# Kernel optimization log

Measured on AMD Instinct MI355X. Metric: run time of the kernel, lower is better.

Reference implementation:

```python
import jax, jax.numpy as jnp
import numpy as np

T = 10          # time_steps
IN_DIM = 784    # 28*28
HID = 256
NCLS = 47
THRESH = 1.0
TAU_MEM = 2.0   # LIF membrane time constant
TAU_OUT = 2.0   # readout EMA time constant


@jax.custom_vjp
def spike_fn(u):
    # Heaviside spike on (v - threshold), surrogate gradient in bwd.
    return (u >= 0.0).astype(u.dtype)

def _spike_fwd(u):
    return spike_fn(u), u

def _spike_bwd(u, g):
    # sigmoid surrogate derivative, slope 4
    s = jax.nn.sigmoid(4.0 * u)
    return (g * 4.0 * s * (1.0 - s),)

spike_fn.defvjp(_spike_fwd, _spike_bwd)


def setup_inputs() -> dict:
    key = jax.random.key(0)
    k1, k2, k3 = jax.random.split(key, 3)
    x = jax.random.uniform(k1, (4096, 1, 28, 28), dtype=jnp.float32)
    W1 = jax.random.normal(k2, (IN_DIM, HID), dtype=jnp.float32) / np.float32(np.sqrt(IN_DIM))
    b1 = jnp.zeros((HID,), jnp.float32)
    Wr = jax.random.normal(k3, (HID, NCLS), dtype=jnp.float32) / np.float32(np.sqrt(HID))
    br = jnp.zeros((NCLS,), jnp.float32)
    return {"x": x, "W1": W1, "b1": b1, "Wr": Wr, "br": br}


def reference(x, W1, b1, Wr, br):
    B = x.shape[0]
    xf = x.reshape(B, -1)  # [B, 784] pixel intensities in [0,1]
    # rate_encode_flat: Bernoulli(p=pixel) spikes per timestep -> [T, B, 784]
    ek = jax.random.key(42)
    seq = (jax.random.uniform(ek, (T, B, IN_DIM), dtype=xf.dtype) < xf[None]).astype(xf.dtype)

    def step(carry, s_t):
        v_hid, v_out = carry
        I_hid = s_t @ W1 + b1                      # [B, HID]
        v_hid = v_hid + (I_hid - v_hid) / TAU_MEM  # leaky integration
        spk = spike_fn(v_hid - THRESH)             # spike emission
        v_hid = v_hid * (1.0 - spk)                # hard reset to 0
        I = spk @ Wr + br                          # [B, NCLS]
        v_out = v_out + (I - v_out) / TAU_OUT      # output EMA
        return (v_hid, v_out), None

    init = (jnp.zeros((B, HID), xf.dtype), jnp.zeros((B, NCLS), xf.dtype))
    (_, v_out), _ = jax.lax.scan(step, init, seq)
    return v_out
```

## Files before the change

### kernel.cpp

```cpp
#include <hip/hip_runtime.h>
#include <stdint.h>


#define T_STEPS 10
#define BATCH   4096
#define IN_DIM  784
#define HID     256
#define NCLS    47
#define NROWS   (T_STEPS * BATCH)
#define KWORDS  25
#define KPAD    800

#define WS_IALL_OFF 0u
#define WS_G_OFF    46039040u
#define WS_W1HI_OFF WS_G_OFF
#define WS_W1MD_OFF (WS_G_OFF + 409600u)
#define WS_W1LO_OFF (WS_G_OFF + 819200u)

typedef __attribute__((ext_vector_type(8))) short    bf16x8;
typedef __attribute__((ext_vector_type(4))) float    f32x4;
typedef __attribute__((ext_vector_type(4))) uint32_t u32x4;

__device__ __forceinline__ uint32_t rotl32(uint32_t x, uint32_t r) {
    return __builtin_amdgcn_alignbit(x, x, 32u - r);
}

__device__ __forceinline__ uint32_t tf_hash(uint32_t lo) {
    const uint32_t ks0 = 0u;
    const uint32_t ks1 = 42u;
    const uint32_t ks2 = 0x1BD11BDAu ^ 0u ^ 42u;
    uint32_t x0 = 0u + ks0;
    uint32_t x1 = lo + ks1;
#define TF_RND(r) { x0 += x1; x1 = rotl32(x1, r); x1 ^= x0; }
    TF_RND(13) TF_RND(15) TF_RND(26) TF_RND(6)
    x0 += ks1; x1 += ks2 + 1u;
    TF_RND(17) TF_RND(29) TF_RND(16) TF_RND(24)
    x0 += ks2; x1 += ks0 + 2u;
    TF_RND(13) TF_RND(15) TF_RND(26) TF_RND(6)
    x0 += ks0; x1 += ks1 + 3u;
    TF_RND(17) TF_RND(29) TF_RND(16) TF_RND(24)
    x0 += ks1; x1 += ks2 + 4u;
    TF_RND(13) TF_RND(15) TF_RND(26) TF_RND(6)
    x0 += ks2; x1 += ks0 + 5u;
#undef TF_RND
    return x0 ^ x1;
}

__global__ __launch_bounds__(256) void splitk_k(
        const float* __restrict__ W1, ushort* __restrict__ hiT,
        ushort* __restrict__ midT, ushort* __restrict__ loT) {
    int n = blockIdx.x;
    for (int k = threadIdx.x; k < KPAD; k += 256) {
        float w = (k < IN_DIM) ? W1[k * HID + n] : 0.0f;
        uint32_t u = __float_as_uint(w);
        uint32_t hb = (u + 0x7FFFu + ((u >> 16) & 1u)) >> 16;
        float hf = __uint_as_float(hb << 16);
        float r1 = w - hf;
        uint32_t u1 = __float_as_uint(r1);
        uint32_t mb = (u1 + 0x7FFFu + ((u1 >> 16) & 1u)) >> 16;
        float mf2 = __uint_as_float(mb << 16);
        float r2 = r1 - mf2;
        uint32_t u2 = __float_as_uint(r2);
        uint32_t lb = (u2 + 0x7FFFu + ((u2 >> 16) & 1u)) >> 16;
        hiT [n * KPAD + k] = (ushort)hb;
        midT[n * KPAD + k] = (ushort)mb;
        loT [n * KPAD + k] = (ushort)lb;
    }
}

#define LDS_A  0
#define LDS_BH 4096
#define LDS_BM 20480
#define LDS_BL 36864

__global__ __launch_bounds__(256, 3) void fused_gemm_k(
        const ushort* __restrict__ hiT, const ushort* __restrict__ midT,
        const ushort* __restrict__ loT, const float* __restrict__ b1,
        const float* __restrict__ x, float* __restrict__ I_all) {
    __shared__ __align__(16) char lds[53248];

    const int tid = threadIdx.x;
    const int l   = tid & 63;
    const int wv  = tid >> 6;
    const int t   = blockIdx.x >> 6;
    const int b0  = (blockIdx.x & 63) << 6;
    const int m0  = blockIdx.x << 6;

    f32x4 acc[4][4] = {};

    const int q   = l >> 4;
    const int sig = q ^ (l & 3) ^ ((l >> 2) & 3);
    const int a_base = LDS_A + ((l & 15) << 6) + (sig << 4);
    const int b_off  = (((wv << 6) + (l & 15)) << 6) + (sig << 4);

    const int er = tid >> 2;
    const int eq = tid & 3;
    const int ea = LDS_A + (er << 6) + ((eq ^ (er & 3) ^ ((er >> 2) & 3)) << 4);
    const int row_b = b0 + er;
    const float* xrow = x + (size_t)row_b * IN_DIM;
    const uint32_t ibase = (uint32_t)(row_b * IN_DIM)
                         + (uint32_t)t * (uint32_t)(BATCH * IN_DIM);

    for (int kw = 0; kw < KWORDS; ++kw) {
        __syncthreads();

#pragma unroll
        for (int i = 0; i < 4; ++i) {
            int s  = (wv << 8) + (i << 6) + l;
            int n  = s >> 2;
            int qs = s & 3;
            int qd = qs ^ (n & 3) ^ ((n >> 2) & 3);
            size_t gb = (size_t)n * (KPAD * 2) + ((size_t)kw << 6) + ((size_t)qd << 4);
            int ldst = ((wv << 8) + (i << 6)) << 4;
            __builtin_amdgcn_global_load_lds(
                (const __attribute__((address_space(1))) void*)((const char*)hiT + gb),
                (__attribute__((address_space(3))) void*)(lds + LDS_BH + ldst),
                16, 0, 0);
            __builtin_amdgcn_global_load_lds(
                (const __attribute__((address_space(1))) void*)((const char*)midT + gb),
                (__attribute__((address_space(3))) void*)(lds + LDS_BM + ldst),
                16, 0, 0);
            __builtin_amdgcn_global_load_lds(
                (const __attribute__((address_space(1))) void*)((const char*)loT + gb),
                (__attribute__((address_space(3))) void*)(lds + LDS_BL + ldst),
                16, 0, 0);
        }

        {
            u32x4 v = {0u, 0u, 0u, 0u};
            if (!(kw == 24 && eq >= 2)) {
                const int k0 = (kw << 5) + (eq << 3);
                float4 xa = *(const float4*)&xrow[k0];
                float4 xb = *(const float4*)&xrow[k0 + 4];
                const uint32_t ib = ibase + (uint32_t)k0;
                uint32_t c0 = ((float)(tf_hash(ib + 0u) >> 9) < xa.x * 8388608.0f) ? 0x3F80u : 0u;
                uint32_t c1 = ((float)(tf_hash(ib + 1u) >> 9) < xa.y * 8388608.0f) ? 0x3F800000u : 0u;
                uint32_t c2 = ((float)(tf_hash(ib + 2u) >> 9) < xa.z * 8388608.0f) ? 0x3F80u : 0u;
                uint32_t c3 = ((float)(tf_hash(ib + 3u) >> 9) < xa.w * 8388608.0f) ? 0x3F800000u : 0u;
                uint32_t c4 = ((float)(tf_hash(ib + 4u) >> 9) < xb.x * 8388608.0f) ? 0x3F80u : 0u;
                uint32_t c5 = ((float)(tf_hash(ib + 5u) >> 9) < xb.y * 8388608.0f) ? 0x3F800000u : 0u;
                uint32_t c6 = ((float)(tf_hash(ib + 6u) >> 9) < xb.z * 8388608.0f) ? 0x3F80u : 0u;
                uint32_t c7 = ((float)(tf_hash(ib + 7u) >> 9) < xb.w * 8388608.0f) ? 0x3F800000u : 0u;
                v.x = c0 | c1;  v.y = c2 | c3;  v.z = c4 | c5;  v.w = c6 | c7;
            }
            *(u32x4*)(lds + ea) = v;
        }

        __syncthreads();

        bf16x8 af[4];
#pragma unroll
        for (int mt = 0; mt < 4; ++mt)
            af[mt] = *(const bf16x8*)(lds + a_base + (mt << 10));
#pragma unroll
        for (int nt = 0; nt < 4; ++nt) {
            bf16x8 bh = *(const bf16x8*)(lds + LDS_BH + b_off + (nt << 10));
            bf16x8 bm = *(const bf16x8*)(lds + LDS_BM + b_off + (nt << 10));
            bf16x8 bl = *(const bf16x8*)(lds + LDS_BL + b_off + (nt << 10));
#pragma unroll
            for (int mt = 0; mt < 4; ++mt) {
                acc[mt][nt] = __builtin_amdgcn_mfma_f32_16x16x32_bf16(af[mt], bh, acc[mt][nt], 0, 0, 0);
                acc[mt][nt] = __builtin_amdgcn_mfma_f32_16x16x32_bf16(af[mt], bm, acc[mt][nt], 0, 0, 0);
                acc[mt][nt] = __builtin_amdgcn_mfma_f32_16x16x32_bf16(af[mt], bl, acc[mt][nt], 0, 0, 0);
            }
        }
    }

    const int c0 = l & 15;
    float b1v[4];
#pragma unroll
    for (int nt = 0; nt < 4; ++nt)
        b1v[nt] = b1[(wv << 6) + (nt << 4) + c0];
#pragma unroll
    for (int mt = 0; mt < 4; ++mt) {
#pragma unroll
        for (int nt = 0; nt < 4; ++nt) {
            int col = (wv << 6) + (nt << 4) + c0;
#pragma unroll
            for (int r = 0; r < 4; ++r) {
                int row = m0 + (mt << 4) + (q << 2) + r;
                I_all[(size_t)row * HID + col] = acc[mt][nt][r] + b1v[nt];
            }
        }
    }
}

__global__ __launch_bounds__(256) void scan_k(
        const float* __restrict__ I_all, float* __restrict__ g) {
    int b = blockIdx.x;
    int h = threadIdx.x;
    const float* p = I_all + ((size_t)b << 8) + h;
    float v = 0.f, ga = 0.f, wt = 0.0009765625f;
#pragma unroll
    for (int t = 0; t < T_STEPS; ++t) {
        float I = p[(size_t)t * BATCH * HID];
        v = v + (I - v) * 0.5f;
        if (v >= 1.0f) { ga += wt; v = 0.f; }
        wt += wt;
    }
    g[(b << 8) + h] = ga;
}

__global__ __launch_bounds__(256) void out_k(
        const float* __restrict__ g, const float* __restrict__ Wr,
        const float* __restrict__ br, float* __restrict__ out) {
    __shared__ float gl[4 * 256];
    int tid = threadIdx.x;
    int b0 = blockIdx.x << 2;
    *(float4*)&gl[tid << 2] = *(const float4*)&g[(b0 << 8) + (tid << 2)];
    __syncthreads();
    int row = tid >> 6;
    int c = tid & 63;
    if (c >= NCLS) return;
    const float* grow = &gl[row << 8];
    float acc = 0.f;
#pragma unroll 4
    for (int h = 0; h < HID; ++h)
        acc = fmaf(grow[h], Wr[h * NCLS + c], acc);
    out[(b0 + row) * NCLS + c] = acc + br[c] * 0.9990234375f;
}

extern "C" void kernel_launch(void* const* d_in, const int* in_sizes, int n_in,
                              void* d_out, int out_size, void* d_ws, size_t ws_size,
                              hipStream_t stream) {
    const float* x  = (const float*)d_in[0];
    const float* W1 = (const float*)d_in[1];
    const float* b1 = (const float*)d_in[2];
    const float* Wr = (const float*)d_in[3];
    const float* br = (const float*)d_in[4];
    float* out = (float*)d_out;

    float*    I_all = (float*)   ((char*)d_ws + WS_IALL_OFF);
    float*    g     = (float*)   ((char*)d_ws + WS_G_OFF);
    ushort*   w1hi  = (ushort*)  ((char*)d_ws + WS_W1HI_OFF);
    ushort*   w1md  = (ushort*)  ((char*)d_ws + WS_W1MD_OFF);
    ushort*   w1lo  = (ushort*)  ((char*)d_ws + WS_W1LO_OFF);

    splitk_k<<<HID, 256, 0, stream>>>(W1, w1hi, w1md, w1lo);
    fused_gemm_k<<<NROWS / 64, 256, 0, stream>>>(w1hi, w1md, w1lo, b1, x, I_all);
    scan_k<<<BATCH, 256, 0, stream>>>(I_all, g);
    out_k<<<BATCH / 4, 256, 0, stream>>>(g, Wr, br, out);
}
```

Baseline: 209.7 us.

## Double-buffer hashed input slab, inline-asm threefry rotates, fuse scan with readout

The GEMM kernel now double-buffers the Bernoulli-encoded A tile in LDS. The hash for the next k-slab is computed while the current slab's MFMAs run, so each iteration still uses two barriers but with less serialization. The threefry rotations use inline v_alignbit asm with precomputed shift amounts, and the zero key additions are dropped. The LIF scan and the readout matmul are merged into one kernel that handles 16 batch rows per block, which removes the g buffer round trip and one launch. In exchange, LDS use grows and occupancy may drop.

Measured after the change: 231.9 us. 1.11x slower.

```diff
diff --git a/kernel.cpp b/kernel.cpp
--- a/kernel.cpp
+++ b/kernel.cpp
@@ -12,37 +12,34 @@
 #define KPAD    800
 
 #define WS_IALL_OFF 0u
-#define WS_G_OFF    46039040u
-#define WS_W1HI_OFF WS_G_OFF
-#define WS_W1MD_OFF (WS_G_OFF + 409600u)
-#define WS_W1LO_OFF (WS_G_OFF + 819200u)
+#define WS_W1HI_OFF 46039040u
+#define WS_W1MD_OFF (46039040u + 409600u)
+#define WS_W1LO_OFF (46039040u + 819200u)
 
 typedef __attribute__((ext_vector_type(8))) short    bf16x8;
 typedef __attribute__((ext_vector_type(4))) float    f32x4;
 typedef __attribute__((ext_vector_type(4))) uint32_t u32x4;
 
-__device__ __forceinline__ uint32_t rotl32(uint32_t x, uint32_t r) {
-    return __builtin_amdgcn_alignbit(x, x, 32u - r);
-}
+#define TF_RND(s32mr) {                                             \
+    x0 += x1;                                                       \
+    asm("v_alignbit_b32 %0, %1, %1, " s32mr : "=v"(x1) : "v"(x1));  \
+    x1 ^= x0; }
 
 __device__ __forceinline__ uint32_t tf_hash(uint32_t lo) {
-    const uint32_t ks0 = 0u;
     const uint32_t ks1 = 42u;
-    const uint32_t ks2 = 0x1BD11BDAu ^ 0u ^ 42u;
-    uint32_t x0 = 0u + ks0;
+    const uint32_t ks2 = 0x1BD11BDAu ^ 42u;
+    uint32_t x0 = 0u;
     uint32_t x1 = lo + ks1;
-#define TF_RND(r) { x0 += x1; x1 = rotl32(x1, r); x1 ^= x0; }
-    TF_RND(13) TF_RND(15) TF_RND(26) TF_RND(6)
+    TF_RND("19") TF_RND("17") TF_RND("6")  TF_RND("26")
     x0 += ks1; x1 += ks2 + 1u;
-    TF_RND(17) TF_RND(29) TF_RND(16) TF_RND(24)
-    x0 += ks2; x1 += ks0 + 2u;
-    TF_RND(13) TF_RND(15) TF_RND(26) TF_RND(6)
-    x0 += ks0; x1 += ks1 + 3u;
-    TF_RND(17) TF_RND(29) TF_RND(16) TF_RND(24)
+    TF_RND("15") TF_RND("3")  TF_RND("16") TF_RND("8")
+    x0 += ks2; x1 += 2u;
+    TF_RND("19") TF_RND("17") TF_RND("6")  TF_RND("26")
+    x1 += ks1 + 3u;
+    TF_RND("15") TF_RND("3")  TF_RND("16") TF_RND("8")
     x0 += ks1; x1 += ks2 + 4u;
-    TF_RND(13) TF_RND(15) TF_RND(26) TF_RND(6)
-    x0 += ks2; x1 += ks0 + 5u;
-#undef TF_RND
+    TF_RND("19") TF_RND("17") TF_RND("6")  TF_RND("26")
+    x0 += ks2; x1 += 5u;
     return x0 ^ x1;
 }
 
@@ -68,16 +65,17 @@
     }
 }
 
-#define LDS_A  0
-#define LDS_BH 4096
-#define LDS_BM 20480
-#define LDS_BL 36864
+#define LDS_A0 0
+#define LDS_A1 4096
+#define LDS_BH 8192
+#define LDS_BM 24576
+#define LDS_BL 40960
 
 __global__ __launch_bounds__(256, 3) void fused_gemm_k(
         const ushort* __restrict__ hiT, const ushort* __restrict__ midT,
         const ushort* __restrict__ loT, const float* __restrict__ b1,
         const float* __restrict__ x, float* __restrict__ I_all) {
-    __shared__ __align__(16) char lds[53248];
+    __shared__ __align__(16) char lds[57344];
 
     const int tid = threadIdx.x;
     const int l   = tid & 63;
@@ -90,16 +88,38 @@
 
     const int q   = l >> 4;
     const int sig = q ^ (l & 3) ^ ((l >> 2) & 3);
-    const int a_base = LDS_A + ((l & 15) << 6) + (sig << 4);
+    const int a_base = ((l & 15) << 6) + (sig << 4);
     const int b_off  = (((wv << 6) + (l & 15)) << 6) + (sig << 4);
 
     const int er = tid >> 2;
     const int eq = tid & 3;
-    const int ea = LDS_A + (er << 6) + ((eq ^ (er & 3) ^ ((er >> 2) & 3)) << 4);
+    const int ea = (er << 6) + ((eq ^ (er & 3) ^ ((er >> 2) & 3)) << 4);
     const int row_b = b0 + er;
     const float* xrow = x + (size_t)row_b * IN_DIM;
     const uint32_t ibase = (uint32_t)(row_b * IN_DIM)
                          + (uint32_t)t * (uint32_t)(BATCH * IN_DIM);
+
+    auto hash_slab = [&](int kwt, char* dst) {
+        u32x4 v = {0u, 0u, 0u, 0u};
+        if (!(kwt == 24 && eq >= 2)) {
+            const int k0 = (kwt << 5) + (eq << 3);
+            float4 xa = *(const float4*)&xrow[k0];
+            float4 xb = *(const float4*)&xrow[k0 + 4];
+            const uint32_t ib = ibase + (uint32_t)k0;
+            uint32_t c0 = ((float)(tf_hash(ib + 0u) >> 9) < xa.x * 8388608.0f) ? 0x3F80u : 0u;
+            uint32_t c1 = ((float)(tf_hash(ib + 1u) >> 9) < xa.y * 8388608.0f) ? 0x3F800000u : 0u;
+            uint32_t c2 = ((float)(tf_hash(ib + 2u) >> 9) < xa.z * 8388608.0f) ? 0x3F80u : 0u;
+            uint32_t c3 = ((float)(tf_hash(ib + 3u) >> 9) < xa.w * 8388608.0f) ? 0x3F800000u : 0u;
+            uint32_t c4 = ((float)(tf_hash(ib + 4u) >> 9) < xb.x * 8388608.0f) ? 0x3F80u : 0u;
+            uint32_t c5 = ((float)(tf_hash(ib + 5u) >> 9) < xb.y * 8388608.0f) ? 0x3F800000u : 0u;
+            uint32_t c6 = ((float)(tf_hash(ib + 6u) >> 9) < xb.z * 8388608.0f) ? 0x3F80u : 0u;
+            uint32_t c7 = ((float)(tf_hash(ib + 7u) >> 9) < xb.w * 8388608.0f) ? 0x3F800000u : 0u;
+            v.x = c0 | c1;  v.y = c2 | c3;  v.z = c4 | c5;  v.w = c6 | c7;
+        }
+        *(u32x4*)dst = v;
+    };
+
+    hash_slab(0, lds + LDS_A0 + ea);
 
     for (int kw = 0; kw < KWORDS; ++kw) {
         __syncthreads();
@@ -126,32 +146,16 @@
                 16, 0, 0);
         }
 
-        {
-            u32x4 v = {0u, 0u, 0u, 0u};
-            if (!(kw == 24 && eq >= 2)) {
-                const int k0 = (kw << 5) + (eq << 3);
-                float4 xa = *(const float4*)&xrow[k0];
-                float4 xb = *(const float4*)&xrow[k0 + 4];
-                const uint32_t ib = ibase + (uint32_t)k0;
-                uint32_t c0 = ((float)(tf_hash(ib + 0u) >> 9) < xa.x * 8388608.0f) ? 0x3F80u : 0u;
-                uint32_t c1 = ((float)(tf_hash(ib + 1u) >> 9) < xa.y * 8388608.0f) ? 0x3F800000u : 0u;
-                uint32_t c2 = ((float)(tf_hash(ib + 2u) >> 9) < xa.z * 8388608.0f) ? 0x3F80u : 0u;
-                uint32_t c3 = ((float)(tf_hash(ib + 3u) >> 9) < xa.w * 8388608.0f) ? 0x3F800000u : 0u;
-                uint32_t c4 = ((float)(tf_hash(ib + 4u) >> 9) < xb.x * 8388608.0f) ? 0x3F80u : 0u;
-                uint32_t c5 = ((float)(tf_hash(ib + 5u) >> 9) < xb.y * 8388608.0f) ? 0x3F800000u : 0u;
-                uint32_t c6 = ((float)(tf_hash(ib + 6u) >> 9) < xb.z * 8388608.0f) ? 0x3F80u : 0u;
-                uint32_t c7 = ((float)(tf_hash(ib + 7u) >> 9) < xb.w * 8388608.0f) ? 0x3F800000u : 0u;
-                v.x = c0 | c1;  v.y = c2 | c3;  v.z = c4 | c5;  v.w = c6 | c7;
-            }
-            *(u32x4*)(lds + ea) = v;
-        }
+        if (kw + 1 < KWORDS)
+            hash_slab(kw + 1, lds + ((kw & 1) ? LDS_A0 : LDS_A1) + ea);
 
         __syncthreads();
 
+        const char* abuf = lds + ((kw & 1) ? LDS_A1 : LDS_A0);
         bf16x8 af[4];
 #pragma unroll
         for (int mt = 0; mt < 4; ++mt)
-            af[mt] = *(const bf16x8*)(lds + a_base + (mt << 10));
+            af[mt] = *(const bf16x8*)(abuf + a_base + (mt << 10));
 #pragma unroll
         for (int nt = 0; nt < 4; ++nt) {
             bf16x8 bh = *(const bf16x8*)(lds + LDS_BH + b_off + (nt << 10));
@@ -185,39 +189,50 @@
     }
 }
 
-__global__ __launch_bounds__(256) void scan_k(
-        const float* __restrict__ I_all, float* __restrict__ g) {
-    int b = blockIdx.x;
-    int h = threadIdx.x;
-    const float* p = I_all + ((size_t)b << 8) + h;
-    float v = 0.f, ga = 0.f, wt = 0.0009765625f;
-#pragma unroll
-    for (int t = 0; t < T_STEPS; ++t) {
-        float I = p[(size_t)t * BATCH * HID];
-        v = v + (I - v) * 0.5f;
-        if (v >= 1.0f) { ga += wt; v = 0.f; }
-        wt += wt;
-    }
-    g[(b << 8) + h] = ga;
-}
-
-__global__ __launch_bounds__(256) void out_k(
-        const float* __restrict__ g, const float* __restrict__ Wr,
+__global__ __launch_bounds__(256) void scanout_k(
+        const float* __restrict__ I_all, const float* __restrict__ Wr,
         const float* __restrict__ br, float* __restrict__ out) {
-    __shared__ float gl[4 * 256];
-    int tid = threadIdx.x;
-    int b0 = blockIdx.x << 2;
-    *(float4*)&gl[tid << 2] = *(const float4*)&g[(b0 << 8) + (tid << 2)];
+    __shared__ float gl[16 * 256];
+    const int tid = threadIdx.x;
+    const int b0  = blockIdx.x << 4;
+
+#pragma unroll 4
+    for (int b = 0; b < 16; ++b) {
+        const float* p = I_all + ((size_t)(b0 + b) << 8) + tid;
+        float v = 0.f, ga = 0.f, wt = 0.0009765625f;
+#pragma unroll
+        for (int t = 0; t < T_STEPS; ++t) {
+            float I = p[(size_t)t * BATCH * HID];
+            v = v + (I - v) * 0.5f;
+            if (v >= 1.0f) { ga += wt; v = 0.f; }
+            wt += wt;
+        }
+        gl[(b << 8) + tid] = ga;
+    }
     __syncthreads();
-    int row = tid >> 6;
-    int c = tid & 63;
+
+    const int wv = tid >> 6;
+    const int c  = tid & 63;
     if (c >= NCLS) return;
-    const float* grow = &gl[row << 8];
-    float acc = 0.f;
-#pragma unroll 4
-    for (int h = 0; h < HID; ++h)
-        acc = fmaf(grow[h], Wr[h * NCLS + c], acc);
-    out[(b0 + row) * NCLS + c] = acc + br[c] * 0.9990234375f;
+    float acc[4] = {0.f, 0.f, 0.f, 0.f};
+    for (int h4 = 0; h4 < 64; ++h4) {
+        float w0 = Wr[((h4 << 2) + 0) * NCLS + c];
+        float w1 = Wr[((h4 << 2) + 1) * NCLS + c];
+        float w2 = Wr[((h4 << 2) + 2) * NCLS + c];
+        float w3 = Wr[((h4 << 2) + 3) * NCLS + c];
+#pragma unroll
+        for (int j = 0; j < 4; ++j) {
+            float4 gg = *(float4*)&gl[(((wv << 2) + j) << 8) + (h4 << 2)];
+            acc[j] = fmaf(gg.x, w0, acc[j]);
+            acc[j] = fmaf(gg.y, w1, acc[j]);
+            acc[j] = fmaf(gg.z, w2, acc[j]);
+            acc[j] = fmaf(gg.w, w3, acc[j]);
+        }
+    }
+    float brv = br[c] * 0.9990234375f;
+#pragma unroll
+    for (int j = 0; j < 4; ++j)
+        out[(b0 + (wv << 2) + j) * NCLS + c] = acc[j] + brv;
 }
 
 extern "C" void kernel_launch(void* const* d_in, const int* in_sizes, int n_in,
@@ -230,14 +245,12 @@
     const float* br = (const float*)d_in[4];
     float* out = (float*)d_out;
 
-    float*    I_all = (float*)   ((char*)d_ws + WS_IALL_OFF);
-    float*    g     = (float*)   ((char*)d_ws + WS_G_OFF);
-    ushort*   w1hi  = (ushort*)  ((char*)d_ws + WS_W1HI_OFF);
-    ushort*   w1md  = (ushort*)  ((char*)d_ws + WS_W1MD_OFF);
-    ushort*   w1lo  = (ushort*)  ((char*)d_ws + WS_W1LO_OFF);
+    float*  I_all = (float*) ((char*)d_ws + WS_IALL_OFF);
+    ushort* w1hi  = (ushort*)((char*)d_ws + WS_W1HI_OFF);
+    ushort* w1md  = (ushort*)((char*)d_ws + WS_W1MD_OFF);
+    ushort* w1lo  = (ushort*)((char*)d_ws + WS_W1LO_OFF);
 
     splitk_k<<<HID, 256, 0, stream>>>(W1, w1hi, w1md, w1lo);
     fused_gemm_k<<<NROWS / 64, 256, 0, stream>>>(w1hi, w1md, w1lo, b1, x, I_all);
-    scan_k<<<BATCH, 256, 0, stream>>>(I_all, g);
-    out_k<<<BATCH / 4, 256, 0, stream>>>(g, Wr, br, out);
-}
+    scanout_k<<<BATCH / 16, 256, 0, stream>>>(I_all, Wr, br, out);
+}
```
